# Optimization experiments

Measured on AMD Instinct MI355X. Metric: run time of the kernel, lower is better.

The kernel has to match this reference:

```python
import jax, jax.numpy as jnp
import numpy as np

B, T, N, H, L = 64, 256, 512, 1024, 2


def setup_inputs() -> dict:
    key = jax.random.key(0)
    ks = jax.random.split(key, 12)
    s = 0.02  # weight init scale
    return {
        "x": jax.random.normal(ks[0], (B, T, N), jnp.float32),
        "h": jax.random.normal(ks[1], (L, B, H), jnp.float32),
        "c": jax.random.normal(ks[2], (L, B, H), jnp.float32),
        # layer 0: input dim N
        "W_ih0": jax.random.normal(ks[3], (4 * H, N), jnp.float32) * s,
        "W_hh0": jax.random.normal(ks[4], (4 * H, H), jnp.float32) * s,
        "b_ih0": jax.random.normal(ks[5], (4 * H,), jnp.float32) * s,
        "b_hh0": jax.random.normal(ks[6], (4 * H,), jnp.float32) * s,
        # layer 1: input dim H
        "W_ih1": jax.random.normal(ks[7], (4 * H, H), jnp.float32) * s,
        "W_hh1": jax.random.normal(ks[8], (4 * H, H), jnp.float32) * s,
        "b_ih1": jax.random.normal(ks[9], (4 * H,), jnp.float32) * s,
        "b_hh1": jax.random.normal(ks[10], (4 * H,), jnp.float32) * s,
    }


def _lstm_cell(x_t, h_l, c_l, Wi, Wh, bi, bh):
    # gates: [B, 4H], torch LSTMCell gate order i, f, g, o
    gates = x_t @ Wi.T + h_l @ Wh.T + bi + bh
    i, f, g, o = jnp.split(gates, 4, axis=-1)
    i, f, o = jax.nn.sigmoid(i), jax.nn.sigmoid(f), jax.nn.sigmoid(o)
    g = jnp.tanh(g)
    c_new = f * c_l + i * g
    h_new = o * jnp.tanh(c_new)
    return h_new, c_new


def reference(x, h, c, W_ih0, W_hh0, b_ih0, b_hh0, W_ih1, W_hh1, b_ih1, b_hh1):
    params = [(W_ih0, W_hh0, b_ih0, b_hh0), (W_ih1, W_hh1, b_ih1, b_hh1)]

    def step(carry, x_t):
        h, c = carry  # each [L, B, H]
        inp = x_t
        new_h, new_c = [], []
        for l, (Wi, Wh, bi, bh) in enumerate(params):
            h_new, c_new = _lstm_cell(inp, h[l], c[l], Wi, Wh, bi, bh)
            new_h.append(h_new)
            new_c.append(c_new)
            inp = h_new
        return (jnp.stack(new_h), jnp.stack(new_c)), inp

    xT = jnp.swapaxes(x, 0, 1)  # [T, B, N]
    (h_final, c_final), outsT = jax.lax.scan(step, (h, c), xT)
    outs = jnp.swapaxes(outsT, 0, 1)  # [B, T, H]
    return outs, h_final, c_final
```

## Files before the change

### kernel.cpp

```cpp
#include <hip/hip_runtime.h>
#include <hip/hip_bf16.h>


#define T_ 256
#define B_ 64
#define N_ 512
#define H_ 1024
#define FH_ 4096
#define NWG_SEQ 256
#define BH_ (B_ * H_)

typedef _Float16 f16;
typedef _Float16 f16x4 __attribute__((ext_vector_type(4)));
typedef _Float16 f16x8 __attribute__((ext_vector_type(8)));
typedef float f32x4 __attribute__((ext_vector_type(4)));
typedef unsigned long long ull;

template <bool V> struct BC { static constexpr bool value = V; };

__device__ __forceinline__ float sigf(float x) { return 1.f / (1.f + __expf(-x)); }
__device__ __forceinline__ float tanhf_fast(float x) { return 1.f - 2.f / (__expf(2.f * x) + 1.f); }

__device__ __forceinline__ void st_u64g(ull* p, ull v) {
  __hip_atomic_store(p, v, __ATOMIC_RELAXED, __HIP_MEMORY_SCOPE_AGENT);
}
__device__ __forceinline__ void st_u32g(unsigned* p, unsigned v) {
  __hip_atomic_store(p, v, __ATOMIC_RELAXED, __HIP_MEMORY_SCOPE_AGENT);
}
__device__ __forceinline__ ull ld_u64g(const ull* p) {
  return __hip_atomic_load(p, __ATOMIC_RELAXED, __HIP_MEMORY_SCOPE_AGENT);
}
__device__ __forceinline__ f16x8 ld_b128_nc(const f16* p) {
  f16x8 r;
  asm volatile("global_load_dwordx4 %0, %1, off sc0 sc1" : "=v"(r) : "v"(p));
  return r;
}
template <bool CACHED>
__device__ __forceinline__ f16x8 ldf(const f16* p) {
  if constexpr (CACHED) return *(const f16x8*)p;
  else return ld_b128_nc(p);
}

__global__ __launch_bounds__(256) void init_all(
    const float* __restrict__ x, const float* __restrict__ h,
    const float* __restrict__ Wih0, const float* __restrict__ bih0, const float* __restrict__ bhh0,
    const float* __restrict__ Whh0, const float* __restrict__ Wih1, const float* __restrict__ Whh1,
    const float* __restrict__ bih1, const float* __restrict__ bhh1,
    f16* __restrict__ xT, f16* __restrict__ wih0, f16* __restrict__ whh0,
    f16* __restrict__ wih1, f16* __restrict__ whh1,
    float* __restrict__ bias0, float* __restrict__ bias1,
    f16* __restrict__ hinit, unsigned* __restrict__ flags)
{
  const int stride = gridDim.x * blockDim.x;
  const int t0 = blockIdx.x * blockDim.x + threadIdx.x;

  for (int i = t0; i < T_ * B_ * N_; i += stride) {
    int n = i & (N_ - 1);
    int tb = i >> 9;
    int b = tb & (B_ - 1);
    int t = tb >> 6;
    xT[i] = (f16)x[((size_t)b * T_ + t) * N_ + n];
  }
  for (int i = t0; i < FH_ * N_; i += stride) wih0[i] = (f16)Wih0[i];
  for (int i = t0; i < FH_ * H_; i += stride) {
    whh0[i] = (f16)Whh0[i];
    wih1[i] = (f16)Wih1[i];
    whh1[i] = (f16)Whh1[i];
  }
  for (int i = t0; i < FH_; i += stride) {
    bias0[i] = bih0[i] + bhh0[i];
    bias1[i] = bih1[i] + bhh1[i];
  }
  for (int i = t0; i < 2 * BH_; i += stride) hinit[i] = (f16)h[i];
  if (t0 < 256) flags[t0] = 0u;
}

__global__ __launch_bounds__(256) void gemm_pre0(
    const f16* __restrict__ xT, const f16* __restrict__ wih0,
    const float* __restrict__ bias0, f16* __restrict__ pre0T)
{
  const int wid = threadIdx.x >> 6;
  const int lane = threadIdx.x & 63;
  const int lr = lane & 15;
  const int lkq = (lane >> 4) << 3;
  const int lrq = (lane >> 4) << 2;

  const int mt = blockIdx.x & 255;
  const int ct = (blockIdx.x >> 8) * 4 + wid;
  const int row0 = mt * 64, col0 = ct * 64;

  f32x4 acc[4][4] = {};
  const f16* Abase = xT + (size_t)row0 * N_;

  #pragma unroll 2
  for (int kk = 0; kk < N_ / 32; ++kk) {
    const int k = kk * 32 + lkq;
    f16x8 a[4], b[4];
    #pragma unroll
    for (int r = 0; r < 4; ++r)
      a[r] = *(const f16x8*)(Abase + (size_t)(r * 16 + lr) * N_ + k);
    #pragma unroll
    for (int cf = 0; cf < 4; ++cf)
      b[cf] = *(const f16x8*)(wih0 + (size_t)(col0 + cf * 16 + lr) * N_ + k);
    #pragma unroll
    for (int r = 0; r < 4; ++r)
      #pragma unroll
      for (int cf = 0; cf < 4; ++cf)
        acc[r][cf] = __builtin_amdgcn_mfma_f32_16x16x32_f16(a[r], b[cf], acc[r][cf], 0, 0, 0);
  }

  #pragma unroll
  for (int r = 0; r < 4; ++r) {
    #pragma unroll
    for (int cf = 0; cf < 4; ++cf) {
      const int col = col0 + cf * 16 + lr;
      const float bv = bias0[col];
      f16x4 pv;
      #pragma unroll
      for (int ri = 0; ri < 4; ++ri) pv[ri] = (f16)(acc[r][cf][ri] + bv);
      *(f16x4*)(pre0T + ((size_t)mt * FH_ + col) * 64 + r * 16 + lrq) = pv;
    }
  }
}

template <bool DEEP>
__global__ __launch_bounds__(256, 1) void lstm_seq(
    const f16* __restrict__ pre0T, const f16* __restrict__ whh0,
    const f16* __restrict__ wih1, const f16* __restrict__ whh1,
    const float* __restrict__ bias1, const f16* __restrict__ hinit,
    const float* __restrict__ cin,
    f16* __restrict__ h0r, f16* __restrict__ h1r,
    float* __restrict__ out, unsigned* __restrict__ flags)
{
  __shared__ __align__(16) float exc[2][4][32][33];
  __shared__ __align__(16) f16 smH[2][32][8];

  const int tid = threadIdx.x;
  const int p = tid >> 6;
  const int lane = tid & 63;
  const int lr = lane & 15;
  const int lq = lane >> 4;
  const int lkq = lq << 3;
  const int lrq = lq << 2;

  const int wg = blockIdx.x;
  const int pod = wg >> 7;
  const int slot = wg & 127;
  const int rs = pod << 5;
  const int ub = slot << 3;
  unsigned* podflags = flags + (pod << 7);

  auto rt = [&](int t) -> size_t { return DEEP ? (size_t)t : (size_t)(t & 7); };

  f16x8 l0w[2][8], l1aw[2][8], l1bw[2][8];
  #pragma unroll
  for (int cf = 0; cf < 2; ++cf) {
    const size_t wr = (size_t)((2 * cf + (lr >> 3)) * H_ + ub + (lr & 7)) * H_;
    #pragma unroll
    for (int j = 0; j < 8; ++j) {
      const int k = (p * 8 + j) * 32 + lkq;
      l0w[cf][j]  = *(const f16x8*)(whh0 + wr + k);
      l1aw[cf][j] = *(const f16x8*)(wih1 + wr + k);
      l1bw[cf][j] = *(const f16x8*)(whh1 + wr + k);
    }
  }

  const int crow = tid & 31;
  const int cu = tid >> 5;
  const size_t cell = (size_t)(rs + crow) * H_ + ub + cu;
  float c0 = cin[cell];
  float c1 = cin[(size_t)BH_ + cell];
  float b1v[4];
  #pragma unroll
  for (int g = 0; g < 4; ++g) b1v[g] = bias1[g * H_ + ub + cu];

  float* outh = out + (size_t)B_ * T_ * H_;
  float* outc = outh + 2 * BH_;

  auto body = [&](auto A0c, auto A1c, int e) {
    constexpr bool A0 = decltype(A0c)::value;
    constexpr bool A1 = decltype(A1c)::value;

    float pf[4];
    if (A0) {
      #pragma unroll
      for (int g = 0; g < 4; ++g)
        pf[g] = (float)pre0T[((size_t)e * FH_ + g * H_ + ub + cu) * 64 + rs + crow];
    }

    if (e > 0 && p == 0) {
      const ull* fp = (const ull*)podflags;
      for (;;) {
        ull v = ld_u64g(&fp[lane]);
        const bool ok = ((unsigned)v >= (unsigned)e) && ((unsigned)(v >> 32) >= (unsigned)e);
        if (__ballot(ok) == ~0ull) break;
        __builtin_amdgcn_s_sleep(1);
      }
    }
    __syncthreads();

    const f16* h0s = ((e == 0) ? hinit : h0r + rt(e - 1) * BH_) + (size_t)rs * H_;
    const f16* h1s = A1 ? (((e == 1) ? hinit + BH_ : h1r + rt(e - 2) * BH_) + (size_t)rs * H_)
                        : (const f16*)nullptr;
    f16x8 a0v[8], a1v[8], c0v[8], c1v[8];
    #pragma unroll
    for (int j = 0; j < 8; ++j) {
      const int k = (p * 8 + j) * 32 + lkq;
      a0v[j] = ldf<DEEP>(h0s + (size_t)lr * H_ + k);
      a1v[j] = ldf<DEEP>(h0s + (size_t)(16 + lr) * H_ + k);
    }
    if (A1) {
      #pragma unroll
      for (int j = 0; j < 8; ++j) {
        const int k = (p * 8 + j) * 32 + lkq;
        c0v[j] = ldf<DEEP>(h1s + (size_t)lr * H_ + k);
        c1v[j] = ldf<DEEP>(h1s + (size_t)(16 + lr) * H_ + k);
      }
    }
    if (!DEEP) {
      asm volatile("s_waitcnt vmcnt(0)" ::: "memory");
      __builtin_amdgcn_sched_barrier(0);
    }

    f32x4 acc0[2][2] = {};
    f32x4 acc1[2][2] = {};
    #pragma unroll
    for (int j = 0; j < 8; ++j) {
      if (A0) {
        #pragma unroll
        for (int cf = 0; cf < 2; ++cf) {
          acc0[cf][0] = __builtin_amdgcn_mfma_f32_16x16x32_f16(a0v[j], l0w[cf][j], acc0[cf][0], 0, 0, 0);
          acc0[cf][1] = __builtin_amdgcn_mfma_f32_16x16x32_f16(a1v[j], l0w[cf][j], acc0[cf][1], 0, 0, 0);
        }
      }
      if (A1) {
        #pragma unroll
        for (int cf = 0; cf < 2; ++cf) {
          acc1[cf][0] = __builtin_amdgcn_mfma_f32_16x16x32_f16(a0v[j], l1aw[cf][j], acc1[cf][0], 0, 0, 0);
          acc1[cf][1] = __builtin_amdgcn_mfma_f32_16x16x32_f16(a1v[j], l1aw[cf][j], acc1[cf][1], 0, 0, 0);
        }
      }
    }
    if (A1) {
      #pragma unroll
      for (int j = 0; j < 8; ++j) {
        #pragma unroll
        for (int cf = 0; cf < 2; ++cf) {
          acc1[cf][0] = __builtin_amdgcn_mfma_f32_16x16x32_f16(c0v[j], l1bw[cf][j], acc1[cf][0], 0, 0, 0);
          acc1[cf][1] = __builtin_amdgcn_mfma_f32_16x16x32_f16(c1v[j], l1bw[cf][j], acc1[cf][1], 0, 0, 0);
        }
      }
    }

    #pragma unroll
    for (int cf = 0; cf < 2; ++cf)
      #pragma unroll
      for (int rf = 0; rf < 2; ++rf)
        #pragma unroll
        for (int ri = 0; ri < 4; ++ri) {
          if (A0) exc[0][p][rf * 16 + lrq + ri][cf * 16 + lr] = acc0[cf][rf][ri];
          if (A1) exc[1][p][rf * 16 + lrq + ri][cf * 16 + lr] = acc1[cf][rf][ri];
        }
    __syncthreads();

    float hn0 = 0.f, cn0 = 0.f, hn1 = 0.f, cn1 = 0.f;
    if (A0) {
      float gv[4];
      #pragma unroll
      for (int g = 0; g < 4; ++g)
        gv[g] = exc[0][0][crow][g * 8 + cu] + exc[0][1][crow][g * 8 + cu]
              + exc[0][2][crow][g * 8 + cu] + exc[0][3][crow][g * 8 + cu] + pf[g];
      cn0 = sigf(gv[1]) * c0 + sigf(gv[0]) * tanhf_fast(gv[2]);
      hn0 = sigf(gv[3]) * tanhf_fast(cn0);
      c0 = cn0;
      smH[0][crow][cu] = (f16)hn0;
    }
    if (A1) {
      float gv[4];
      #pragma unroll
      for (int g = 0; g < 4; ++g)
        gv[g] = exc[1][0][crow][g * 8 + cu] + exc[1][1][crow][g * 8 + cu]
              + exc[1][2][crow][g * 8 + cu] + exc[1][3][crow][g * 8 + cu] + b1v[g];
      cn1 = sigf(gv[1]) * c1 + sigf(gv[0]) * tanhf_fast(gv[2]);
      hn1 = sigf(gv[3]) * tanhf_fast(cn1);
      c1 = cn1;
      smH[1][crow][cu] = (f16)hn1;
    }
    __syncthreads();

    if (A0 && p == 0) {
      const int row = lane >> 1, half = lane & 1;
      ull v = *(const ull*)&smH[0][row][half * 4];
      st_u64g((ull*)(h0r + rt(e) * BH_ + (size_t)(rs + row) * H_ + ub + half * 4), v);
    }
    if (A1 && p == 1) {
      const int row = lane >> 1, half = lane & 1;
      ull v = *(const ull*)&smH[1][row][half * 4];
      st_u64g((ull*)(h1r + rt(e - 1) * BH_ + (size_t)(rs + row) * H_ + ub + half * 4), v);
    }
    asm volatile("s_waitcnt vmcnt(0)" ::: "memory");
    __syncthreads();
    if (tid == 0) st_u32g(&podflags[slot], (unsigned)(e + 1));

    if (A0 && e == T_ - 1) { outh[cell] = hn0; outc[cell] = cn0; }
    if (A1) {
      out[(size_t)(rs + crow) * (T_ * H_) + (size_t)(e - 1) * H_ + ub + cu] = hn1;
      if (e == T_) { outh[BH_ + cell] = hn1; outc[BH_ + cell] = cn1; }
    }
  };

  body(BC<true>{}, BC<false>{}, 0);
  for (int e = 1; e < T_; ++e) body(BC<true>{}, BC<true>{}, e);
  body(BC<false>{}, BC<true>{}, T_);
}

extern "C" void kernel_launch(void* const* d_in, const int* in_sizes, int n_in,
                              void* d_out, int out_size, void* d_ws, size_t ws_size,
                              hipStream_t stream)
{
  const float* x    = (const float*)d_in[0];
  const float* h    = (const float*)d_in[1];
  const float* c    = (const float*)d_in[2];
  const float* Wih0 = (const float*)d_in[3];
  const float* Whh0 = (const float*)d_in[4];
  const float* bih0 = (const float*)d_in[5];
  const float* bhh0 = (const float*)d_in[6];
  const float* Wih1 = (const float*)d_in[7];
  const float* Whh1 = (const float*)d_in[8];
  const float* bih1 = (const float*)d_in[9];
  const float* bhh1 = (const float*)d_in[10];

  char* w = (char*)d_ws;
  size_t off = 0;
  auto carve = [&](size_t bytes) -> char* {
    char* ptr = w + off;
    off = (off + bytes + 255) & ~(size_t)255;
    return ptr;
  };
  f16*   pre0T = (f16*)  carve((size_t)T_ * B_ * FH_ * 2);
  f16*   xT    = (f16*)  carve((size_t)T_ * B_ * N_ * 2);
  f16*   wih0  = (f16*)  carve((size_t)FH_ * N_ * 2);
  f16*   whh0  = (f16*)  carve((size_t)FH_ * H_ * 2);
  f16*   wih1  = (f16*)  carve((size_t)FH_ * H_ * 2);
  f16*   whh1  = (f16*)  carve((size_t)FH_ * H_ * 2);
  float* bias0 = (float*)carve((size_t)FH_ * 4);
  float* bias1 = (float*)carve((size_t)FH_ * 4);
  f16*   hinit = (f16*)  carve((size_t)2 * BH_ * 2);
  f16*   h0s   = (f16*)  carve((size_t)8 * BH_ * 2);
  f16*   h1s   = (f16*)  carve((size_t)8 * BH_ * 2);
  unsigned* flags = (unsigned*)carve(256 * 4);
  const size_t base_end = off;
  f16*   h0ring = (f16*) carve((size_t)T_ * BH_ * 2);
  f16*   h1ring = (f16*) carve((size_t)T_ * BH_ * 2);
  const bool deep = (off <= ws_size);
  if (base_end > ws_size) return;

  init_all<<<2048, 256, 0, stream>>>(x, h, Wih0, bih0, bhh0, Whh0, Wih1, Whh1, bih1, bhh1,
                                     xT, wih0, whh0, wih1, whh1, bias0, bias1, hinit, flags);
  gemm_pre0<<<4096, 256, 0, stream>>>(xT, wih0, bias0, pre0T);
  if (deep)
    lstm_seq<true><<<NWG_SEQ, 256, 0, stream>>>(pre0T, whh0, wih1, whh1, bias1, hinit,
                                                (const float*)c, h0ring, h1ring,
                                                (float*)d_out, flags);
  else
    lstm_seq<false><<<NWG_SEQ, 256, 0, stream>>>(pre0T, whh0, wih1, whh1, bias1, hinit,
                                                 (const float*)c, h0s, h1s,
                                                 (float*)d_out, flags);
}
```

Measured before the change: 2.063 ms.

## Split per-layer flags and wait per K-chunk to overlap layer-0 recurrence

Replaces the single per-step flag barrier with separate flag arrays for layer 0 and layer 1. In deep mode each wave waits only for the producer workgroups of the K-chunk it is about to consume, and loads the next chunk while running MFMAs on the current one. Layer-0 h is published and flagged before the layer-1 recurrent part runs, so the layer-0 critical path no longer waits on layer-1 work. The K layout is reinterleaved so that chunks line up with producer groups. This adds more flag polling and an extra block barrier per step, and it depends on subtle memory-ordering behaviour.

```diff
diff --git a/kernel.cpp b/kernel.cpp
--- a/kernel.cpp
+++ b/kernel.cpp
@@ -34,11 +34,6 @@
   f16x8 r;
   asm volatile("global_load_dwordx4 %0, %1, off sc0 sc1" : "=v"(r) : "v"(p));
   return r;
-}
-template <bool CACHED>
-__device__ __forceinline__ f16x8 ldf(const f16* p) {
-  if constexpr (CACHED) return *(const f16x8*)p;
-  else return ld_b128_nc(p);
 }
 
 __global__ __launch_bounds__(256) void init_all(
@@ -72,7 +67,7 @@
     bias1[i] = bih1[i] + bhh1[i];
   }
   for (int i = t0; i < 2 * BH_; i += stride) hinit[i] = (f16)h[i];
-  if (t0 < 256) flags[t0] = 0u;
+  if (t0 < 512) flags[t0] = 0u;
 }
 
 __global__ __launch_bounds__(256) void gemm_pre0(
@@ -148,7 +143,8 @@
   const int slot = wg & 127;
   const int rs = pod << 5;
   const int ub = slot << 3;
-  unsigned* podflags = flags + (pod << 7);
+  unsigned* f0p = flags + (pod << 7);
+  unsigned* f1p = flags + 256 + (pod << 7);
 
   auto rt = [&](int t) -> size_t { return DEEP ? (size_t)t : (size_t)(t & 7); };
 
@@ -157,11 +153,11 @@
   for (int cf = 0; cf < 2; ++cf) {
     const size_t wr = (size_t)((2 * cf + (lr >> 3)) * H_ + ub + (lr & 7)) * H_;
     #pragma unroll
-    for (int j = 0; j < 8; ++j) {
-      const int k = (p * 8 + j) * 32 + lkq;
-      l0w[cf][j]  = *(const f16x8*)(whh0 + wr + k);
-      l1aw[cf][j] = *(const f16x8*)(wih1 + wr + k);
-      l1bw[cf][j] = *(const f16x8*)(whh1 + wr + k);
+    for (int ch = 0; ch < 8; ++ch) {
+      const int k = ch * 128 + p * 32 + lkq;
+      l0w[cf][ch]  = *(const f16x8*)(whh0 + wr + k);
+      l1aw[cf][ch] = *(const f16x8*)(wih1 + wr + k);
+      l1bw[cf][ch] = *(const f16x8*)(whh1 + wr + k);
     }
   }
 
@@ -177,6 +173,29 @@
   float* outh = out + (size_t)B_ * T_ * H_;
   float* outc = outh + 2 * BH_;
 
+  auto wchunk = [&](int ch, unsigned tgt) {
+    if (tgt == 0u) return;
+    const ull* fp = (const ull*)f0p;
+    const int idx = 8 * ch + (lane & 7);
+    for (;;) {
+      ull v = ld_u64g(&fp[idx]);
+      const bool ok = ((unsigned)v >= tgt) && ((unsigned)(v >> 32) >= tgt);
+      if (__ballot(ok) == ~0ull) break;
+      __builtin_amdgcn_s_sleep(1);
+    }
+    asm volatile("" ::: "memory");
+  };
+  auto waitwide = [&](const unsigned* base, unsigned tgt) {
+    const ull* fp = (const ull*)base;
+    for (;;) {
+      ull v = ld_u64g(&fp[lane]);
+      const bool ok = ((unsigned)v >= tgt) && ((unsigned)(v >> 32) >= tgt);
+      if (__ballot(ok) == ~0ull) break;
+      __builtin_amdgcn_s_sleep(1);
+    }
+    asm volatile("" ::: "memory");
+  };
+
   auto body = [&](auto A0c, auto A1c, int e) {
     constexpr bool A0 = decltype(A0c)::value;
     constexpr bool A1 = decltype(A1c)::value;
@@ -188,82 +207,84 @@
         pf[g] = (float)pre0T[((size_t)e * FH_ + g * H_ + ub + cu) * 64 + rs + crow];
     }
 
-    if (e > 0 && p == 0) {
-      const ull* fp = (const ull*)podflags;
-      for (;;) {
-        ull v = ld_u64g(&fp[lane]);
-        const bool ok = ((unsigned)v >= (unsigned)e) && ((unsigned)(v >> 32) >= (unsigned)e);
-        if (__ballot(ok) == ~0ull) break;
-        __builtin_amdgcn_s_sleep(1);
-      }
-    }
-    __syncthreads();
+    if (!DEEP && e >= 7) waitwide(f1p, (unsigned)(e - 6));
 
     const f16* h0s = ((e == 0) ? hinit : h0r + rt(e - 1) * BH_) + (size_t)rs * H_;
-    const f16* h1s = A1 ? (((e == 1) ? hinit + BH_ : h1r + rt(e - 2) * BH_) + (size_t)rs * H_)
-                        : (const f16*)nullptr;
-    f16x8 a0v[8], a1v[8], c0v[8], c1v[8];
-    #pragma unroll
-    for (int j = 0; j < 8; ++j) {
-      const int k = (p * 8 + j) * 32 + lkq;
-      a0v[j] = ldf<DEEP>(h0s + (size_t)lr * H_ + k);
-      a1v[j] = ldf<DEEP>(h0s + (size_t)(16 + lr) * H_ + k);
-    }
-    if (A1) {
-      #pragma unroll
-      for (int j = 0; j < 8; ++j) {
-        const int k = (p * 8 + j) * 32 + lkq;
-        c0v[j] = ldf<DEEP>(h1s + (size_t)lr * H_ + k);
-        c1v[j] = ldf<DEEP>(h1s + (size_t)(16 + lr) * H_ + k);
-      }
-    }
-    if (!DEEP) {
+
+    f32x4 acc0[2][2] = {};
+    f32x4 acc1[2][2] = {};
+
+    if constexpr (DEEP) {
+      f16x8 ca0, ca1, pa0, pa1;
+      wchunk(0, (unsigned)e);
+      ca0 = *(const f16x8*)(h0s + (size_t)lr * H_ + (p * 32 + lkq));
+      ca1 = *(const f16x8*)(h0s + (size_t)(16 + lr) * H_ + (p * 32 + lkq));
+      #pragma unroll
+      for (int ch = 0; ch < 8; ++ch) {
+        if (ch < 7) {
+          wchunk(ch + 1, (unsigned)e);
+          const int k = (ch + 1) * 128 + p * 32 + lkq;
+          pa0 = *(const f16x8*)(h0s + (size_t)lr * H_ + k);
+          pa1 = *(const f16x8*)(h0s + (size_t)(16 + lr) * H_ + k);
+        }
+        if (A0) {
+          #pragma unroll
+          for (int cf = 0; cf < 2; ++cf) {
+            acc0[cf][0] = __builtin_amdgcn_mfma_f32_16x16x32_f16(ca0, l0w[cf][ch], acc0[cf][0], 0, 0, 0);
+            acc0[cf][1] = __builtin_amdgcn_mfma_f32_16x16x32_f16(ca1, l0w[cf][ch], acc0[cf][1], 0, 0, 0);
+          }
+        }
+        if (A1) {
+          #pragma unroll
+          for (int cf = 0; cf < 2; ++cf) {
+            acc1[cf][0] = __builtin_amdgcn_mfma_f32_16x16x32_f16(ca0, l1aw[cf][ch], acc1[cf][0], 0, 0, 0);
+            acc1[cf][1] = __builtin_amdgcn_mfma_f32_16x16x32_f16(ca1, l1aw[cf][ch], acc1[cf][1], 0, 0, 0);
+          }
+        }
+        if (ch < 7) { ca0 = pa0; ca1 = pa1; }
+      }
+    } else {
+      if (e > 0) waitwide(f0p, (unsigned)e);
+      f16x8 a0v[8], a1v[8];
+      #pragma unroll
+      for (int ch = 0; ch < 8; ++ch) {
+        const int k = ch * 128 + p * 32 + lkq;
+        a0v[ch] = ld_b128_nc(h0s + (size_t)lr * H_ + k);
+        a1v[ch] = ld_b128_nc(h0s + (size_t)(16 + lr) * H_ + k);
+      }
       asm volatile("s_waitcnt vmcnt(0)" ::: "memory");
       __builtin_amdgcn_sched_barrier(0);
-    }
-
-    f32x4 acc0[2][2] = {};
-    f32x4 acc1[2][2] = {};
-    #pragma unroll
-    for (int j = 0; j < 8; ++j) {
-      if (A0) {
+      #pragma unroll
+      for (int ch = 0; ch < 8; ++ch) {
+        if (A0) {
+          #pragma unroll
+          for (int cf = 0; cf < 2; ++cf) {
+            acc0[cf][0] = __builtin_amdgcn_mfma_f32_16x16x32_f16(a0v[ch], l0w[cf][ch], acc0[cf][0], 0, 0, 0);
+            acc0[cf][1] = __builtin_amdgcn_mfma_f32_16x16x32_f16(a1v[ch], l0w[cf][ch], acc0[cf][1], 0, 0, 0);
+          }
+        }
+        if (A1) {
+          #pragma unroll
+          for (int cf = 0; cf < 2; ++cf) {
+            acc1[cf][0] = __builtin_amdgcn_mfma_f32_16x16x32_f16(a0v[ch], l1aw[cf][ch], acc1[cf][0], 0, 0, 0);
+            acc1[cf][1] = __builtin_amdgcn_mfma_f32_16x16x32_f16(a1v[ch], l1aw[cf][ch], acc1[cf][1], 0, 0, 0);
+          }
+        }
+      }
+    }
+
+    if (A0) {
+      #pragma unroll
+      for (int cf = 0; cf < 2; ++cf)
         #pragma unroll
-        for (int cf = 0; cf < 2; ++cf) {
-          acc0[cf][0] = __builtin_amdgcn_mfma_f32_16x16x32_f16(a0v[j], l0w[cf][j], acc0[cf][0], 0, 0, 0);
-          acc0[cf][1] = __builtin_amdgcn_mfma_f32_16x16x32_f16(a1v[j], l0w[cf][j], acc0[cf][1], 0, 0, 0);
-        }
-      }
-      if (A1) {
-        #pragma unroll
-        for (int cf = 0; cf < 2; ++cf) {
-          acc1[cf][0] = __builtin_amdgcn_mfma_f32_16x16x32_f16(a0v[j], l1aw[cf][j], acc1[cf][0], 0, 0, 0);
-          acc1[cf][1] = __builtin_amdgcn_mfma_f32_16x16x32_f16(a1v[j], l1aw[cf][j], acc1[cf][1], 0, 0, 0);
-        }
-      }
-    }
-    if (A1) {
-      #pragma unroll
-      for (int j = 0; j < 8; ++j) {
-        #pragma unroll
-        for (int cf = 0; cf < 2; ++cf) {
-          acc1[cf][0] = __builtin_amdgcn_mfma_f32_16x16x32_f16(c0v[j], l1bw[cf][j], acc1[cf][0], 0, 0, 0);
-          acc1[cf][1] = __builtin_amdgcn_mfma_f32_16x16x32_f16(c1v[j], l1bw[cf][j], acc1[cf][1], 0, 0, 0);
-        }
-      }
-    }
-
-    #pragma unroll
-    for (int cf = 0; cf < 2; ++cf)
-      #pragma unroll
-      for (int rf = 0; rf < 2; ++rf)
-        #pragma unroll
-        for (int ri = 0; ri < 4; ++ri) {
-          if (A0) exc[0][p][rf * 16 + lrq + ri][cf * 16 + lr] = acc0[cf][rf][ri];
-          if (A1) exc[1][p][rf * 16 + lrq + ri][cf * 16 + lr] = acc1[cf][rf][ri];
-        }
+        for (int rf = 0; rf < 2; ++rf)
+          #pragma unroll
+          for (int ri = 0; ri < 4; ++ri)
+            exc[0][p][rf * 16 + lrq + ri][cf * 16 + lr] = acc0[cf][rf][ri];
+    }
     __syncthreads();
 
-    float hn0 = 0.f, cn0 = 0.f, hn1 = 0.f, cn1 = 0.f;
+    float hn0 = 0.f, cn0 = 0.f;
     if (A0) {
       float gv[4];
       #pragma unroll
@@ -275,6 +296,54 @@
       c0 = cn0;
       smH[0][crow][cu] = (f16)hn0;
     }
+    __syncthreads();
+
+    if (A0 && p == 0) {
+      const int row = lane >> 1, half = lane & 1;
+      ull v = *(const ull*)&smH[0][row][half * 4];
+      st_u64g((ull*)(h0r + rt(e) * BH_ + (size_t)(rs + row) * H_ + ub + half * 4), v);
+      asm volatile("s_waitcnt vmcnt(0)" ::: "memory");
+      if (lane == 0) st_u32g(&f0p[slot], (unsigned)(e + 1));
+    }
+
+    if (A1) {
+      if (e >= 2) waitwide(f1p, (unsigned)e);
+      const f16* h1s = ((e == 1) ? hinit + BH_ : h1r + rt(e - 2) * BH_) + (size_t)rs * H_;
+      f16x8 c0v[8], c1v[8];
+      #pragma unroll
+      for (int ch = 0; ch < 8; ++ch) {
+        const int k = ch * 128 + p * 32 + lkq;
+        if constexpr (DEEP) {
+          c0v[ch] = *(const f16x8*)(h1s + (size_t)lr * H_ + k);
+          c1v[ch] = *(const f16x8*)(h1s + (size_t)(16 + lr) * H_ + k);
+        } else {
+          c0v[ch] = ld_b128_nc(h1s + (size_t)lr * H_ + k);
+          c1v[ch] = ld_b128_nc(h1s + (size_t)(16 + lr) * H_ + k);
+        }
+      }
+      if (!DEEP) {
+        asm volatile("s_waitcnt vmcnt(0)" ::: "memory");
+        __builtin_amdgcn_sched_barrier(0);
+      }
+      #pragma unroll
+      for (int ch = 0; ch < 8; ++ch) {
+        #pragma unroll
+        for (int cf = 0; cf < 2; ++cf) {
+          acc1[cf][0] = __builtin_amdgcn_mfma_f32_16x16x32_f16(c0v[ch], l1bw[cf][ch], acc1[cf][0], 0, 0, 0);
+          acc1[cf][1] = __builtin_amdgcn_mfma_f32_16x16x32_f16(c1v[ch], l1bw[cf][ch], acc1[cf][1], 0, 0, 0);
+        }
+      }
+      #pragma unroll
+      for (int cf = 0; cf < 2; ++cf)
+        #pragma unroll
+        for (int rf = 0; rf < 2; ++rf)
+          #pragma unroll
+          for (int ri = 0; ri < 4; ++ri)
+            exc[1][p][rf * 16 + lrq + ri][cf * 16 + lr] = acc1[cf][rf][ri];
+    }
+    __syncthreads();
+
+    float hn1 = 0.f, cn1 = 0.f;
     if (A1) {
       float gv[4];
       #pragma unroll
@@ -288,19 +357,13 @@
     }
     __syncthreads();
 
-    if (A0 && p == 0) {
-      const int row = lane >> 1, half = lane & 1;
-      ull v = *(const ull*)&smH[0][row][half * 4];
-      st_u64g((ull*)(h0r + rt(e) * BH_ + (size_t)(rs + row) * H_ + ub + half * 4), v);
-    }
     if (A1 && p == 1) {
       const int row = lane >> 1, half = lane & 1;
       ull v = *(const ull*)&smH[1][row][half * 4];
       st_u64g((ull*)(h1r + rt(e - 1) * BH_ + (size_t)(rs + row) * H_ + ub + half * 4), v);
-    }
-    asm volatile("s_waitcnt vmcnt(0)" ::: "memory");
-    __syncthreads();
-    if (tid == 0) st_u32g(&podflags[slot], (unsigned)(e + 1));
+      asm volatile("s_waitcnt vmcnt(0)" ::: "memory");
+      if (lane == 0) st_u32g(&f1p[slot], (unsigned)(e + 1));
+    }
 
     if (A0 && e == T_ - 1) { outh[cell] = hn0; outc[cell] = cn0; }
     if (A1) {
@@ -348,7 +411,7 @@
   f16*   hinit = (f16*)  carve((size_t)2 * BH_ * 2);
   f16*   h0s   = (f16*)  carve((size_t)8 * BH_ * 2);
   f16*   h1s   = (f16*)  carve((size_t)8 * BH_ * 2);
-  unsigned* flags = (unsigned*)carve(256 * 4);
+  unsigned* flags = (unsigned*)carve(512 * 4);
   const size_t base_end = off;
   f16*   h0ring = (f16*) carve((size_t)T_ * BH_ * 2);
   f16*   h1ring = (f16*) carve((size_t)T_ * BH_ * 2);
```

After: 2.363 ms. +14.5%, slower.

## Split per-step barrier into separate layer-0 and layer-1 flag chains

Applied to the files above, without the earlier changes.

Replaces the single per-step pod flag with two flag arrays, one per layer. Layer-0 h is published and flagged as soon as it is computed, and layer-1 work waits only on the layer-1 flags. This lets layer-0 of the next step start before layer-1 of the current step finishes across the pod, aiming to shorten the critical path of the wavefront recurrence. In exchange each step has more __syncthreads and two spin-waits, and the layer-1 operand loads are now issued after the layer-0 compute instead of alongside it.

```diff
diff --git a/kernel.cpp b/kernel.cpp
--- a/kernel.cpp
+++ b/kernel.cpp
@@ -34,11 +34,6 @@
   f16x8 r;
   asm volatile("global_load_dwordx4 %0, %1, off sc0 sc1" : "=v"(r) : "v"(p));
   return r;
-}
-template <bool CACHED>
-__device__ __forceinline__ f16x8 ldf(const f16* p) {
-  if constexpr (CACHED) return *(const f16x8*)p;
-  else return ld_b128_nc(p);
 }
 
 __global__ __launch_bounds__(256) void init_all(
@@ -72,7 +67,7 @@
     bias1[i] = bih1[i] + bhh1[i];
   }
   for (int i = t0; i < 2 * BH_; i += stride) hinit[i] = (f16)h[i];
-  if (t0 < 256) flags[t0] = 0u;
+  if (t0 < 512) flags[t0] = 0u;
 }
 
 __global__ __launch_bounds__(256) void gemm_pre0(
@@ -148,7 +143,8 @@
   const int slot = wg & 127;
   const int rs = pod << 5;
   const int ub = slot << 3;
-  unsigned* podflags = flags + (pod << 7);
+  unsigned* f0p = flags + (pod << 7);
+  unsigned* f1p = flags + 256 + (pod << 7);
 
   auto rt = [&](int t) -> size_t { return DEEP ? (size_t)t : (size_t)(t & 7); };
 
@@ -177,6 +173,17 @@
   float* outh = out + (size_t)B_ * T_ * H_;
   float* outc = outh + 2 * BH_;
 
+  auto waitwide = [&](const unsigned* base, unsigned tgt) {
+    const ull* fp = (const ull*)base;
+    for (;;) {
+      ull v = ld_u64g(&fp[lane]);
+      const bool ok = ((unsigned)v >= tgt) && ((unsigned)(v >> 32) >= tgt);
+      if (__ballot(ok) == ~0ull) break;
+      __builtin_amdgcn_s_sleep(1);
+    }
+    asm volatile("" ::: "memory");
+  };
+
   auto body = [&](auto A0c, auto A1c, int e) {
     constexpr bool A0 = decltype(A0c)::value;
     constexpr bool A1 = decltype(A1c)::value;
@@ -188,33 +195,23 @@
         pf[g] = (float)pre0T[((size_t)e * FH_ + g * H_ + ub + cu) * 64 + rs + crow];
     }
 
-    if (e > 0 && p == 0) {
-      const ull* fp = (const ull*)podflags;
-      for (;;) {
-        ull v = ld_u64g(&fp[lane]);
-        const bool ok = ((unsigned)v >= (unsigned)e) && ((unsigned)(v >> 32) >= (unsigned)e);
-        if (__ballot(ok) == ~0ull) break;
-        __builtin_amdgcn_s_sleep(1);
-      }
+    if (p == 0) {
+      if (!DEEP && e >= 7) waitwide(f1p, (unsigned)(e - 6));
+      if (e > 0) waitwide(f0p, (unsigned)e);
     }
     __syncthreads();
 
     const f16* h0s = ((e == 0) ? hinit : h0r + rt(e - 1) * BH_) + (size_t)rs * H_;
-    const f16* h1s = A1 ? (((e == 1) ? hinit + BH_ : h1r + rt(e - 2) * BH_) + (size_t)rs * H_)
-                        : (const f16*)nullptr;
-    f16x8 a0v[8], a1v[8], c0v[8], c1v[8];
+    f16x8 a0v[8], a1v[8];
     #pragma unroll
     for (int j = 0; j < 8; ++j) {
       const int k = (p * 8 + j) * 32 + lkq;
-      a0v[j] = ldf<DEEP>(h0s + (size_t)lr * H_ + k);
-      a1v[j] = ldf<DEEP>(h0s + (size_t)(16 + lr) * H_ + k);
-    }
-    if (A1) {
-      #pragma unroll
-      for (int j = 0; j < 8; ++j) {
-        const int k = (p * 8 + j) * 32 + lkq;
-        c0v[j] = ldf<DEEP>(h1s + (size_t)lr * H_ + k);
-        c1v[j] = ldf<DEEP>(h1s + (size_t)(16 + lr) * H_ + k);
+      if constexpr (DEEP) {
+        a0v[j] = *(const f16x8*)(h0s + (size_t)lr * H_ + k);
+        a1v[j] = *(const f16x8*)(h0s + (size_t)(16 + lr) * H_ + k);
+      } else {
+        a0v[j] = ld_b128_nc(h0s + (size_t)lr * H_ + k);
+        a1v[j] = ld_b128_nc(h0s + (size_t)(16 + lr) * H_ + k);
       }
     }
     if (!DEEP) {
@@ -222,48 +219,26 @@
       __builtin_amdgcn_sched_barrier(0);
     }
 
-    f32x4 acc0[2][2] = {};
-    f32x4 acc1[2][2] = {};
-    #pragma unroll
-    for (int j = 0; j < 8; ++j) {
-      if (A0) {
+    float hn0 = 0.f, cn0 = 0.f;
+    if (A0) {
+      f32x4 acc0[2][2] = {};
+      #pragma unroll
+      for (int j = 0; j < 8; ++j)
         #pragma unroll
         for (int cf = 0; cf < 2; ++cf) {
           acc0[cf][0] = __builtin_amdgcn_mfma_f32_16x16x32_f16(a0v[j], l0w[cf][j], acc0[cf][0], 0, 0, 0);
           acc0[cf][1] = __builtin_amdgcn_mfma_f32_16x16x32_f16(a1v[j], l0w[cf][j], acc0[cf][1], 0, 0, 0);
         }
-      }
-      if (A1) {
-        #pragma unroll
-        for (int cf = 0; cf < 2; ++cf) {
-          acc1[cf][0] = __builtin_amdgcn_mfma_f32_16x16x32_f16(a0v[j], l1aw[cf][j], acc1[cf][0], 0, 0, 0);
-          acc1[cf][1] = __builtin_amdgcn_mfma_f32_16x16x32_f16(a1v[j], l1aw[cf][j], acc1[cf][1], 0, 0, 0);
-        }
-      }
-    }
-    if (A1) {
-      #pragma unroll
-      for (int j = 0; j < 8; ++j) {
-        #pragma unroll
-        for (int cf = 0; cf < 2; ++cf) {
-          acc1[cf][0] = __builtin_amdgcn_mfma_f32_16x16x32_f16(c0v[j], l1bw[cf][j], acc1[cf][0], 0, 0, 0);
-          acc1[cf][1] = __builtin_amdgcn_mfma_f32_16x16x32_f16(c1v[j], l1bw[cf][j], acc1[cf][1], 0, 0, 0);
-        }
-      }
-    }
-
-    #pragma unroll
-    for (int cf = 0; cf < 2; ++cf)
-      #pragma unroll
-      for (int rf = 0; rf < 2; ++rf)
-        #pragma unroll
-        for (int ri = 0; ri < 4; ++ri) {
-          if (A0) exc[0][p][rf * 16 + lrq + ri][cf * 16 + lr] = acc0[cf][rf][ri];
-          if (A1) exc[1][p][rf * 16 + lrq + ri][cf * 16 + lr] = acc1[cf][rf][ri];
-        }
+      #pragma unroll
+      for (int cf = 0; cf < 2; ++cf)
+        #pragma unroll
+        for (int rf = 0; rf < 2; ++rf)
+          #pragma unroll
+          for (int ri = 0; ri < 4; ++ri)
+            exc[0][p][rf * 16 + lrq + ri][cf * 16 + lr] = acc0[cf][rf][ri];
+    }
     __syncthreads();
 
-    float hn0 = 0.f, cn0 = 0.f, hn1 = 0.f, cn1 = 0.f;
     if (A0) {
       float gv[4];
       #pragma unroll
@@ -275,7 +250,64 @@
       c0 = cn0;
       smH[0][crow][cu] = (f16)hn0;
     }
+    __syncthreads();
+
+    if (A0 && p == 0) {
+      const int row = lane >> 1, half = lane & 1;
+      ull v = *(const ull*)&smH[0][row][half * 4];
+      st_u64g((ull*)(h0r + rt(e) * BH_ + (size_t)(rs + row) * H_ + ub + half * 4), v);
+      asm volatile("s_waitcnt vmcnt(0)" ::: "memory");
+      if (lane == 0) st_u32g(&f0p[slot], (unsigned)(e + 1));
+    }
+
+    float hn1 = 0.f, cn1 = 0.f;
     if (A1) {
+      if (p == 0 && e >= 2) waitwide(f1p, (unsigned)e);
+      __syncthreads();
+
+      const f16* h1s = ((e == 1) ? hinit + BH_ : h1r + rt(e - 2) * BH_) + (size_t)rs * H_;
+      f16x8 c0v[8], c1v[8];
+      #pragma unroll
+      for (int j = 0; j < 8; ++j) {
+        const int k = (p * 8 + j) * 32 + lkq;
+        if constexpr (DEEP) {
+          c0v[j] = *(const f16x8*)(h1s + (size_t)lr * H_ + k);
+          c1v[j] = *(const f16x8*)(h1s + (size_t)(16 + lr) * H_ + k);
+        } else {
+          c0v[j] = ld_b128_nc(h1s + (size_t)lr * H_ + k);
+          c1v[j] = ld_b128_nc(h1s + (size_t)(16 + lr) * H_ + k);
+        }
+      }
+
+      f32x4 acc1[2][2] = {};
+      #pragma unroll
+      for (int j = 0; j < 8; ++j)
+        #pragma unroll
+        for (int cf = 0; cf < 2; ++cf) {
+          acc1[cf][0] = __builtin_amdgcn_mfma_f32_16x16x32_f16(a0v[j], l1aw[cf][j], acc1[cf][0], 0, 0, 0);
+          acc1[cf][1] = __builtin_amdgcn_mfma_f32_16x16x32_f16(a1v[j], l1aw[cf][j], acc1[cf][1], 0, 0, 0);
+        }
+      if (!DEEP) {
+        asm volatile("s_waitcnt vmcnt(0)" ::: "memory");
+        __builtin_amdgcn_sched_barrier(0);
+      }
+      #pragma unroll
+      for (int j = 0; j < 8; ++j)
+        #pragma unroll
+        for (int cf = 0; cf < 2; ++cf) {
+          acc1[cf][0] = __builtin_amdgcn_mfma_f32_16x16x32_f16(c0v[j], l1bw[cf][j], acc1[cf][0], 0, 0, 0);
+          acc1[cf][1] = __builtin_amdgcn_mfma_f32_16x16x32_f16(c1v[j], l1bw[cf][j], acc1[cf][1], 0, 0, 0);
+        }
+
+      #pragma unroll
+      for (int cf = 0; cf < 2; ++cf)
+        #pragma unroll
+        for (int rf = 0; rf < 2; ++rf)
+          #pragma unroll
+          for (int ri = 0; ri < 4; ++ri)
+            exc[1][p][rf * 16 + lrq + ri][cf * 16 + lr] = acc1[cf][rf][ri];
+      __syncthreads();
+
       float gv[4];
       #pragma unroll
       for (int g = 0; g < 4; ++g)
@@ -285,22 +317,16 @@
       hn1 = sigf(gv[3]) * tanhf_fast(cn1);
       c1 = cn1;
       smH[1][crow][cu] = (f16)hn1;
-    }
-    __syncthreads();
-
-    if (A0 && p == 0) {
-      const int row = lane >> 1, half = lane & 1;
-      ull v = *(const ull*)&smH[0][row][half * 4];
-      st_u64g((ull*)(h0r + rt(e) * BH_ + (size_t)(rs + row) * H_ + ub + half * 4), v);
-    }
-    if (A1 && p == 1) {
-      const int row = lane >> 1, half = lane & 1;
-      ull v = *(const ull*)&smH[1][row][half * 4];
-      st_u64g((ull*)(h1r + rt(e - 1) * BH_ + (size_t)(rs + row) * H_ + ub + half * 4), v);
-    }
-    asm volatile("s_waitcnt vmcnt(0)" ::: "memory");
-    __syncthreads();
-    if (tid == 0) st_u32g(&podflags[slot], (unsigned)(e + 1));
+      __syncthreads();
+
+      if (p == 1) {
+        const int row = lane >> 1, half = lane & 1;
+        ull v = *(const ull*)&smH[1][row][half * 4];
+        st_u64g((ull*)(h1r + rt(e - 1) * BH_ + (size_t)(rs + row) * H_ + ub + half * 4), v);
+        asm volatile("s_waitcnt vmcnt(0)" ::: "memory");
+        if (lane == 0) st_u32g(&f1p[slot], (unsigned)(e + 1));
+      }
+    }
 
     if (A0 && e == T_ - 1) { outh[cell] = hn0; outc[cell] = cn0; }
     if (A1) {
@@ -348,7 +374,7 @@
   f16*   hinit = (f16*)  carve((size_t)2 * BH_ * 2);
   f16*   h0s   = (f16*)  carve((size_t)8 * BH_ * 2);
   f16*   h1s   = (f16*)  carve((size_t)8 * BH_ * 2);
-  unsigned* flags = (unsigned*)carve(256 * 4);
+  unsigned* flags = (unsigned*)carve(512 * 4);
   const size_t base_end = off;
   f16*   h0ring = (f16*) carve((size_t)T_ * BH_ * 2);
   f16*   h1ring = (f16*) carve((size_t)T_ * BH_ * 2);
```

Result: faster. 1.944 ms (-5.8%).

## Split batch into two alternating phases with deferred flag publication per workgroup

Applied to the files above, without the earlier changes.

Each of the 256 workgroups now owns 4 hidden units across the whole batch, not 8 units for half the batch, and runs two half-batch phases alternately with separate flag arrays. The ready flag for one phase is published only after the next phase's loads have finished. The goal is to hide the cross-workgroup synchronisation latency of one half-batch behind the other half's compute. This halves the MFMA work per barrier and leaves half the threads idle in the gate math. It also doubles the number of flag waits and barriers per timestep.

```diff
diff --git a/kernel.cpp b/kernel.cpp
--- a/kernel.cpp
+++ b/kernel.cpp
@@ -34,11 +34,6 @@
   f16x8 r;
   asm volatile("global_load_dwordx4 %0, %1, off sc0 sc1" : "=v"(r) : "v"(p));
   return r;
-}
-template <bool CACHED>
-__device__ __forceinline__ f16x8 ldf(const f16* p) {
-  if constexpr (CACHED) return *(const f16x8*)p;
-  else return ld_b128_nc(p);
 }
 
 __global__ __launch_bounds__(256) void init_all(
@@ -72,7 +67,7 @@
     bias1[i] = bih1[i] + bhh1[i];
   }
   for (int i = t0; i < 2 * BH_; i += stride) hinit[i] = (f16)h[i];
-  if (t0 < 256) flags[t0] = 0u;
+  if (t0 < 512) flags[t0] = 0u;
 }
 
 __global__ __launch_bounds__(256) void gemm_pre0(
@@ -132,8 +127,8 @@
     f16* __restrict__ h0r, f16* __restrict__ h1r,
     float* __restrict__ out, unsigned* __restrict__ flags)
 {
-  __shared__ __align__(16) float exc[2][4][32][33];
-  __shared__ __align__(16) f16 smH[2][32][8];
+  __shared__ __align__(16) float exc[2][4][32][17];
+  __shared__ __align__(16) f16 smH[2][32][4];
 
   const int tid = threadIdx.x;
   const int p = tid >> 6;
@@ -143,33 +138,35 @@
   const int lkq = lq << 3;
   const int lrq = lq << 2;
 
-  const int wg = blockIdx.x;
-  const int pod = wg >> 7;
-  const int slot = wg & 127;
-  const int rs = pod << 5;
-  const int ub = slot << 3;
-  unsigned* podflags = flags + (pod << 7);
+  const int slot = blockIdx.x;
+  const int ub = slot << 2;
+  unsigned* fA = flags;
+  unsigned* fB = flags + 256;
 
   auto rt = [&](int t) -> size_t { return DEEP ? (size_t)t : (size_t)(t & 7); };
 
-  f16x8 l0w[2][8], l1aw[2][8], l1bw[2][8];
-  #pragma unroll
-  for (int cf = 0; cf < 2; ++cf) {
-    const size_t wr = (size_t)((2 * cf + (lr >> 3)) * H_ + ub + (lr & 7)) * H_;
+  f16x8 l0w[8], l1aw[8], l1bw[8];
+  {
+    const size_t wr = (size_t)((lr >> 2) * H_ + ub + (lr & 3)) * H_;
     #pragma unroll
     for (int j = 0; j < 8; ++j) {
       const int k = (p * 8 + j) * 32 + lkq;
-      l0w[cf][j]  = *(const f16x8*)(whh0 + wr + k);
-      l1aw[cf][j] = *(const f16x8*)(wih1 + wr + k);
-      l1bw[cf][j] = *(const f16x8*)(whh1 + wr + k);
-    }
-  }
-
+      l0w[j]  = *(const f16x8*)(whh0 + wr + k);
+      l1aw[j] = *(const f16x8*)(wih1 + wr + k);
+      l1bw[j] = *(const f16x8*)(whh1 + wr + k);
+    }
+  }
+
+  const bool act = (tid < 128);
   const int crow = tid & 31;
-  const int cu = tid >> 5;
-  const size_t cell = (size_t)(rs + crow) * H_ + ub + cu;
-  float c0 = cin[cell];
-  float c1 = cin[(size_t)BH_ + cell];
+  const int cu = (tid >> 5) & 3;
+  float c0A = 0.f, c1A = 0.f, c0B = 0.f, c1B = 0.f;
+  if (act) {
+    c0A = cin[(size_t)crow * H_ + ub + cu];
+    c0B = cin[(size_t)(32 + crow) * H_ + ub + cu];
+    c1A = cin[(size_t)BH_ + (size_t)crow * H_ + ub + cu];
+    c1B = cin[(size_t)BH_ + (size_t)(32 + crow) * H_ + ub + cu];
+  }
   float b1v[4];
   #pragma unroll
   for (int g = 0; g < 4; ++g) b1v[g] = bias1[g * H_ + ub + cu];
@@ -177,141 +174,155 @@
   float* outh = out + (size_t)B_ * T_ * H_;
   float* outc = outh + 2 * BH_;
 
-  auto body = [&](auto A0c, auto A1c, int e) {
+  unsigned* pend_ptr = nullptr;
+  unsigned pend_val = 0;
+
+  auto phase = [&](auto A0c, auto A1c, int P, int e, unsigned* fP,
+                   float& rc0, float& rc1) {
     constexpr bool A0 = decltype(A0c)::value;
     constexpr bool A1 = decltype(A1c)::value;
+    const int rs = P << 5;
 
     float pf[4];
-    if (A0) {
+    if (A0 && act) {
       #pragma unroll
       for (int g = 0; g < 4; ++g)
         pf[g] = (float)pre0T[((size_t)e * FH_ + g * H_ + ub + cu) * 64 + rs + crow];
     }
 
-    if (e > 0 && p == 0) {
-      const ull* fp = (const ull*)podflags;
+    if (e > 0 && p < 2) {
+      const ull* fp = (const ull*)fP + (size_t)p * 64;
+      const unsigned tgt = (unsigned)e;
       for (;;) {
         ull v = ld_u64g(&fp[lane]);
-        const bool ok = ((unsigned)v >= (unsigned)e) && ((unsigned)(v >> 32) >= (unsigned)e);
-        if (__ballot(ok) == ~0ull) break;
+        if (__ballot(((unsigned)v >= tgt) && ((unsigned)(v >> 32) >= tgt)) == ~0ull) break;
         __builtin_amdgcn_s_sleep(1);
       }
+      asm volatile("" ::: "memory");
     }
     __syncthreads();
 
     const f16* h0s = ((e == 0) ? hinit : h0r + rt(e - 1) * BH_) + (size_t)rs * H_;
-    const f16* h1s = A1 ? (((e == 1) ? hinit + BH_ : h1r + rt(e - 2) * BH_) + (size_t)rs * H_)
-                        : (const f16*)nullptr;
-    f16x8 a0v[8], a1v[8], c0v[8], c1v[8];
+    f16x8 a[2][8];
     #pragma unroll
     for (int j = 0; j < 8; ++j) {
       const int k = (p * 8 + j) * 32 + lkq;
-      a0v[j] = ldf<DEEP>(h0s + (size_t)lr * H_ + k);
-      a1v[j] = ldf<DEEP>(h0s + (size_t)(16 + lr) * H_ + k);
-    }
+      if constexpr (DEEP) {
+        a[0][j] = *(const f16x8*)(h0s + (size_t)lr * H_ + k);
+        a[1][j] = *(const f16x8*)(h0s + (size_t)(16 + lr) * H_ + k);
+      } else {
+        a[0][j] = ld_b128_nc(h0s + (size_t)lr * H_ + k);
+        a[1][j] = ld_b128_nc(h0s + (size_t)(16 + lr) * H_ + k);
+      }
+    }
+    f16x8 d[2][8];
     if (A1) {
+      const f16* h1s = ((e == 1) ? hinit + BH_ : h1r + rt(e - 2) * BH_) + (size_t)rs * H_;
       #pragma unroll
       for (int j = 0; j < 8; ++j) {
         const int k = (p * 8 + j) * 32 + lkq;
-        c0v[j] = ldf<DEEP>(h1s + (size_t)lr * H_ + k);
-        c1v[j] = ldf<DEEP>(h1s + (size_t)(16 + lr) * H_ + k);
-      }
-    }
-    if (!DEEP) {
-      asm volatile("s_waitcnt vmcnt(0)" ::: "memory");
-      __builtin_amdgcn_sched_barrier(0);
-    }
-
-    f32x4 acc0[2][2] = {};
-    f32x4 acc1[2][2] = {};
-    #pragma unroll
-    for (int j = 0; j < 8; ++j) {
-      if (A0) {
-        #pragma unroll
-        for (int cf = 0; cf < 2; ++cf) {
-          acc0[cf][0] = __builtin_amdgcn_mfma_f32_16x16x32_f16(a0v[j], l0w[cf][j], acc0[cf][0], 0, 0, 0);
-          acc0[cf][1] = __builtin_amdgcn_mfma_f32_16x16x32_f16(a1v[j], l0w[cf][j], acc0[cf][1], 0, 0, 0);
+        if constexpr (DEEP) {
+          d[0][j] = *(const f16x8*)(h1s + (size_t)lr * H_ + k);
+          d[1][j] = *(const f16x8*)(h1s + (size_t)(16 + lr) * H_ + k);
+        } else {
+          d[0][j] = ld_b128_nc(h1s + (size_t)lr * H_ + k);
+          d[1][j] = ld_b128_nc(h1s + (size_t)(16 + lr) * H_ + k);
         }
       }
-      if (A1) {
-        #pragma unroll
-        for (int cf = 0; cf < 2; ++cf) {
-          acc1[cf][0] = __builtin_amdgcn_mfma_f32_16x16x32_f16(a0v[j], l1aw[cf][j], acc1[cf][0], 0, 0, 0);
-          acc1[cf][1] = __builtin_amdgcn_mfma_f32_16x16x32_f16(a1v[j], l1aw[cf][j], acc1[cf][1], 0, 0, 0);
-        }
-      }
-    }
-    if (A1) {
+    }
+    asm volatile("s_waitcnt vmcnt(0)" ::: "memory");
+    __syncthreads();
+    if (tid == 0 && pend_ptr) st_u32g(pend_ptr, pend_val);
+    pend_ptr = fP + slot;
+    pend_val = (unsigned)(e + 1);
+
+    if (A0) {
+      f32x4 acc0[2] = {};
       #pragma unroll
       for (int j = 0; j < 8; ++j) {
-        #pragma unroll
-        for (int cf = 0; cf < 2; ++cf) {
-          acc1[cf][0] = __builtin_amdgcn_mfma_f32_16x16x32_f16(c0v[j], l1bw[cf][j], acc1[cf][0], 0, 0, 0);
-          acc1[cf][1] = __builtin_amdgcn_mfma_f32_16x16x32_f16(c1v[j], l1bw[cf][j], acc1[cf][1], 0, 0, 0);
-        }
-      }
-    }
-
-    #pragma unroll
-    for (int cf = 0; cf < 2; ++cf)
+        acc0[0] = __builtin_amdgcn_mfma_f32_16x16x32_f16(a[0][j], l0w[j], acc0[0], 0, 0, 0);
+        acc0[1] = __builtin_amdgcn_mfma_f32_16x16x32_f16(a[1][j], l0w[j], acc0[1], 0, 0, 0);
+      }
       #pragma unroll
       for (int rf = 0; rf < 2; ++rf)
         #pragma unroll
-        for (int ri = 0; ri < 4; ++ri) {
-          if (A0) exc[0][p][rf * 16 + lrq + ri][cf * 16 + lr] = acc0[cf][rf][ri];
-          if (A1) exc[1][p][rf * 16 + lrq + ri][cf * 16 + lr] = acc1[cf][rf][ri];
-        }
+        for (int ri = 0; ri < 4; ++ri)
+          exc[0][p][rf * 16 + lrq + ri][lr] = acc0[rf][ri];
+    }
+    if (A1) {
+      f32x4 acc1[2] = {};
+      #pragma unroll
+      for (int j = 0; j < 8; ++j) {
+        acc1[0] = __builtin_amdgcn_mfma_f32_16x16x32_f16(a[0][j], l1aw[j], acc1[0], 0, 0, 0);
+        acc1[1] = __builtin_amdgcn_mfma_f32_16x16x32_f16(a[1][j], l1aw[j], acc1[1], 0, 0, 0);
+      }
+      #pragma unroll
+      for (int j = 0; j < 8; ++j) {
+        acc1[0] = __builtin_amdgcn_mfma_f32_16x16x32_f16(d[0][j], l1bw[j], acc1[0], 0, 0, 0);
+        acc1[1] = __builtin_amdgcn_mfma_f32_16x16x32_f16(d[1][j], l1bw[j], acc1[1], 0, 0, 0);
+      }
+      #pragma unroll
+      for (int rf = 0; rf < 2; ++rf)
+        #pragma unroll
+        for (int ri = 0; ri < 4; ++ri)
+          exc[1][p][rf * 16 + lrq + ri][lr] = acc1[rf][ri];
+    }
     __syncthreads();
 
     float hn0 = 0.f, cn0 = 0.f, hn1 = 0.f, cn1 = 0.f;
-    if (A0) {
-      float gv[4];
-      #pragma unroll
-      for (int g = 0; g < 4; ++g)
-        gv[g] = exc[0][0][crow][g * 8 + cu] + exc[0][1][crow][g * 8 + cu]
-              + exc[0][2][crow][g * 8 + cu] + exc[0][3][crow][g * 8 + cu] + pf[g];
-      cn0 = sigf(gv[1]) * c0 + sigf(gv[0]) * tanhf_fast(gv[2]);
-      hn0 = sigf(gv[3]) * tanhf_fast(cn0);
-      c0 = cn0;
-      smH[0][crow][cu] = (f16)hn0;
-    }
-    if (A1) {
-      float gv[4];
-      #pragma unroll
-      for (int g = 0; g < 4; ++g)
-        gv[g] = exc[1][0][crow][g * 8 + cu] + exc[1][1][crow][g * 8 + cu]
-              + exc[1][2][crow][g * 8 + cu] + exc[1][3][crow][g * 8 + cu] + b1v[g];
-      cn1 = sigf(gv[1]) * c1 + sigf(gv[0]) * tanhf_fast(gv[2]);
-      hn1 = sigf(gv[3]) * tanhf_fast(cn1);
-      c1 = cn1;
-      smH[1][crow][cu] = (f16)hn1;
+    if (act) {
+      if (A0) {
+        float gv[4];
+        #pragma unroll
+        for (int g = 0; g < 4; ++g)
+          gv[g] = exc[0][0][crow][g * 4 + cu] + exc[0][1][crow][g * 4 + cu]
+                + exc[0][2][crow][g * 4 + cu] + exc[0][3][crow][g * 4 + cu] + pf[g];
+        cn0 = sigf(gv[1]) * rc0 + sigf(gv[0]) * tanhf_fast(gv[2]);
+        hn0 = sigf(gv[3]) * tanhf_fast(cn0);
+        rc0 = cn0;
+        smH[0][crow][cu] = (f16)hn0;
+      }
+      if (A1) {
+        float gv[4];
+        #pragma unroll
+        for (int g = 0; g < 4; ++g)
+          gv[g] = exc[1][0][crow][g * 4 + cu] + exc[1][1][crow][g * 4 + cu]
+                + exc[1][2][crow][g * 4 + cu] + exc[1][3][crow][g * 4 + cu] + b1v[g];
+        cn1 = sigf(gv[1]) * rc1 + sigf(gv[0]) * tanhf_fast(gv[2]);
+        hn1 = sigf(gv[3]) * tanhf_fast(cn1);
+        rc1 = cn1;
+        smH[1][crow][cu] = (f16)hn1;
+      }
     }
     __syncthreads();
 
-    if (A0 && p == 0) {
-      const int row = lane >> 1, half = lane & 1;
-      ull v = *(const ull*)&smH[0][row][half * 4];
-      st_u64g((ull*)(h0r + rt(e) * BH_ + (size_t)(rs + row) * H_ + ub + half * 4), v);
-    }
-    if (A1 && p == 1) {
-      const int row = lane >> 1, half = lane & 1;
-      ull v = *(const ull*)&smH[1][row][half * 4];
-      st_u64g((ull*)(h1r + rt(e - 1) * BH_ + (size_t)(rs + row) * H_ + ub + half * 4), v);
-    }
-    asm volatile("s_waitcnt vmcnt(0)" ::: "memory");
-    __syncthreads();
-    if (tid == 0) st_u32g(&podflags[slot], (unsigned)(e + 1));
-
-    if (A0 && e == T_ - 1) { outh[cell] = hn0; outc[cell] = cn0; }
-    if (A1) {
-      out[(size_t)(rs + crow) * (T_ * H_) + (size_t)(e - 1) * H_ + ub + cu] = hn1;
-      if (e == T_) { outh[BH_ + cell] = hn1; outc[BH_ + cell] = cn1; }
+    if (A0 && p == 0 && lane < 32) {
+      ull v = *(const ull*)&smH[0][lane][0];
+      st_u64g((ull*)(h0r + rt(e) * BH_ + (size_t)(rs + lane) * H_ + ub), v);
+    }
+    if (A1 && p == 1 && lane < 32) {
+      ull v = *(const ull*)&smH[1][lane][0];
+      st_u64g((ull*)(h1r + rt(e - 1) * BH_ + (size_t)(rs + lane) * H_ + ub), v);
+    }
+
+    if (act) {
+      const size_t cell = (size_t)(rs + crow) * H_ + ub + cu;
+      if (A1) {
+        out[(size_t)(rs + crow) * (T_ * H_) + (size_t)(e - 1) * H_ + ub + cu] = hn1;
+        if (e == T_) { outh[BH_ + cell] = hn1; outc[BH_ + cell] = cn1; }
+      }
+      if (A0 && e == T_ - 1) { outh[cell] = hn0; outc[cell] = cn0; }
     }
   };
 
-  body(BC<true>{}, BC<false>{}, 0);
-  for (int e = 1; e < T_; ++e) body(BC<true>{}, BC<true>{}, e);
-  body(BC<false>{}, BC<true>{}, T_);
+  phase(BC<true>{}, BC<false>{}, 0, 0, fA, c0A, c1A);
+  phase(BC<true>{}, BC<false>{}, 1, 0, fB, c0B, c1B);
+  for (int e = 1; e < T_; ++e) {
+    phase(BC<true>{}, BC<true>{}, 0, e, fA, c0A, c1A);
+    phase(BC<true>{}, BC<true>{}, 1, e, fB, c0B, c1B);
+  }
+  phase(BC<false>{}, BC<true>{}, 0, T_, fA, c0A, c1A);
+  phase(BC<false>{}, BC<true>{}, 1, T_, fB, c0B, c1B);
 }
 
 extern "C" void kernel_launch(void* const* d_in, const int* in_sizes, int n_in,
@@ -348,7 +359,7 @@
   f16*   hinit = (f16*)  carve((size_t)2 * BH_ * 2);
   f16*   h0s   = (f16*)  carve((size_t)8 * BH_ * 2);
   f16*   h1s   = (f16*)  carve((size_t)8 * BH_ * 2);
-  unsigned* flags = (unsigned*)carve(256 * 4);
+  unsigned* flags = (unsigned*)carve(512 * 4);
   const size_t base_end = off;
   f16*   h0ring = (f16*) carve((size_t)T_ * BH_ * 2);
   f16*   h1ring = (f16*) carve((size_t)T_ * BH_ * 2);
```

New measurement: 3.134 ms. 51.9% more time.
